# Kernel optimization log

Measured on AMD Instinct MI355X. Metric: run time of the kernel, lower is better.

The kernel has to match this reference:

```python
import jax, jax.numpy as jnp
import numpy as np

D = 256   # d_model
KG = 64   # KG_dim
B, N = 8, 512
EPS = 1e-5

def setup_inputs() -> dict:
    key = jax.random.key(0)
    ks = jax.random.split(key, 20)
    s = 0.05
    return {
        "vectors": jax.random.normal(ks[0], (B, N, D), jnp.float32),
        "KG_matrix": jax.random.normal(ks[1], (B, N, N, KG), jnp.float32),
        "Wq": jax.random.normal(ks[2], (D, D), jnp.float32) * s,
        "bq": jnp.zeros((D,), jnp.float32),
        "Wk": jax.random.normal(ks[3], (D, D), jnp.float32) * s,
        "bk": jnp.zeros((D,), jnp.float32),
        "Wv": jax.random.normal(ks[4], (D, D), jnp.float32) * s,
        "bv": jnp.zeros((D,), jnp.float32),
        "Wkg": jax.random.normal(ks[5], (KG, KG), jnp.float32) * s,
        "bkg": jnp.zeros((KG,), jnp.float32),
        "fc_w": jax.random.normal(ks[6], (2 * D + KG,), jnp.float32) * s,
        "fc_b": jnp.zeros((), jnp.float32),
        "ln_g": jnp.ones((D,), jnp.float32),
        "ln_b": jnp.zeros((D,), jnp.float32),
        "W1": jax.random.normal(ks[7], (D, D), jnp.float32) * s,
        "b1": jnp.zeros((D,), jnp.float32),
        "W2": jax.random.normal(ks[8], (D, D), jnp.float32) * s,
        "b2": jnp.zeros((D,), jnp.float32),
        "Wo": jax.random.normal(ks[9], (D, D), jnp.float32) * s,  # out_proj (unused in fwd, kept for parity)
        "bo": jnp.zeros((D,), jnp.float32),
    }

def reference(vectors, KG_matrix, Wq, bq, Wk, bk, Wv, bv, Wkg, bkg,
              fc_w, fc_b, ln_g, ln_b, W1, b1, W2, b2, Wo, bo):
    # projections + relu activation (self.activation == relu)
    q = jax.nn.relu(vectors @ Wq + bq)          # [B,N,D]
    k = jax.nn.relu(vectors @ Wk + bk)          # [B,N,D]
    v = jax.nn.relu(vectors @ Wv + bv)          # [B,N,D]
    kg = jax.nn.relu(KG_matrix @ Wkg + bkg)     # [B,N,N,KG]

    # fc over concat([q_i, k_j, kg_ij]) decomposed: score_ij = q_i.wq + k_j.wk + kg_ij.wkg + b
    wq_p, wk_p, wkg_p = fc_w[:D], fc_w[D:2 * D], fc_w[2 * D:]
    sq = q @ wq_p                               # [B,N]
    sk = k @ wk_p                               # [B,N]
    skg = jnp.einsum('bijc,c->bij', kg, wkg_p)  # [B,N,N]
    scores = sq[:, :, None] + sk[:, None, :] + skg + fc_b

    attn_weights = jax.nn.softmax(jax.nn.leaky_relu(scores), axis=-1)  # [B,N,N]
    attn_output = jnp.einsum('bij,bjd->bid', attn_weights, v)          # [B,N,D]

    src = v + attn_output  # dropout = identity at inference
    # LayerNorm
    mu = jnp.mean(src, axis=-1, keepdims=True)
    var = jnp.var(src, axis=-1, keepdims=True)
    src2 = (src - mu) * jax.lax.rsqrt(var + EPS) * ln_g + ln_b
    # FFN with leaky_relu (as in the torch code)
    src2 = jax.nn.leaky_relu(src2 @ W1 + b1) @ W2 + b2
    return src + src2
```

## Files before the change

### kernel.cpp

```cpp
#include <hip/hip_runtime.h>
#include <hip/hip_bf16.h>

#define DD 256
#define NJ 512
#define KGC 64

__device__ inline float wave_reduce_sum(float v) {
  #pragma unroll
  for (int off = 32; off > 0; off >>= 1) v += __shfl_xor(v, off, 64);
  return v;
}
__device__ inline float wave_reduce_max(float v) {
  #pragma unroll
  for (int off = 32; off > 0; off >>= 1) v = fmaxf(v, __shfl_xor(v, off, 64));
  return v;
}

__global__ __launch_bounds__(256) void k_qkv(
    const float* __restrict__ vec,
    const float* __restrict__ Wq, const float* __restrict__ bq,
    const float* __restrict__ Wk, const float* __restrict__ bk,
    const float* __restrict__ Wv, const float* __restrict__ bv,
    const float* __restrict__ fc_w,
    float* __restrict__ v_out, float* __restrict__ sq_out, float* __restrict__ sk_out)
{
  const int R = 8;
  const int r0 = blockIdx.x * R;
  const int tid = threadIdx.x;
  const int lane = tid & 63, wid = tid >> 6;

  __shared__ float sx[R * DD];
  __shared__ float redq[R][4], redk[R][4];

  for (int idx = tid; idx < R * DD; idx += 256)
    sx[idx] = vec[(size_t)r0 * DD + idx];
  __syncthreads();

  const int d = tid;
  float aq[R], ak[R], av[R];
  const float bqd = bq[d], bkd = bk[d], bvd = bv[d];
  #pragma unroll
  for (int r = 0; r < R; r++) { aq[r] = bqd; ak[r] = bkd; av[r] = bvd; }

  for (int k = 0; k < DD; k++) {
    float wq = Wq[k * DD + d], wk = Wk[k * DD + d], wv = Wv[k * DD + d];
    #pragma unroll
    for (int r = 0; r < R; r++) {
      float x = sx[r * DD + k];
      aq[r] = fmaf(x, wq, aq[r]);
      ak[r] = fmaf(x, wk, ak[r]);
      av[r] = fmaf(x, wv, av[r]);
    }
  }

  const float fq = fc_w[d], fk = fc_w[DD + d];
  #pragma unroll
  for (int r = 0; r < R; r++) {
    float vq = fmaxf(aq[r], 0.f) * fq;
    float vk = fmaxf(ak[r], 0.f) * fk;
    vq = wave_reduce_sum(vq);
    vk = wave_reduce_sum(vk);
    if (lane == 0) { redq[r][wid] = vq; redk[r][wid] = vk; }
    v_out[(size_t)(r0 + r) * DD + d] = fmaxf(av[r], 0.f);
  }
  __syncthreads();
  if (tid < R) {
    sq_out[r0 + tid] = redq[tid][0] + redq[tid][1] + redq[tid][2] + redq[tid][3];
  } else if (tid < 2 * R) {
    int r = tid - R;
    sk_out[r0 + r] = redk[r][0] + redk[r][1] + redk[r][2] + redk[r][3];
  }
}

__global__ __launch_bounds__(512) void k_attn(
    const float* __restrict__ KG,
    const float* __restrict__ Wkg, const float* __restrict__ bkg,
    const float* __restrict__ fc_w, const float* __restrict__ fc_b,
    const float* __restrict__ sq, const float* __restrict__ sk,
    const float* __restrict__ v, float* __restrict__ src_out)
{
  const int IT = 4;
  const int row0 = blockIdx.x * IT;
  const int b = row0 >> 9;
  const int tid = threadIdx.x;
  const int lane = tid & 63, wid = tid >> 6;

  __shared__ float sw[IT][NJ];
  __shared__ float smax[8], ssum[8];
  __shared__ float sacc[512];

  const float* wkgp = fc_w + 2 * DD;
  const float fcb = fc_b[0];
  const int j = tid;
  const float skj = sk[b * NJ + j];

  #pragma unroll 1
  for (int ii = 0; ii < IT; ii++) {
    const int i = row0 + ii;
    const float* kgrow = KG + ((size_t)i * NJ + j) * KGC;
    float y[KGC];
    #pragma unroll
    for (int c = 0; c < KGC; c++) y[c] = bkg[c];

    #pragma unroll 1
    for (int cp = 0; cp < KGC; cp += 8) {
      float4 x0 = *(const float4*)(kgrow + cp);
      float4 x1 = *(const float4*)(kgrow + cp + 4);
      float x[8] = {x0.x, x0.y, x0.z, x0.w, x1.x, x1.y, x1.z, x1.w};
      #pragma unroll
      for (int u = 0; u < 8; u++) {
        #pragma unroll
        for (int c = 0; c < KGC; c++)
          y[c] = fmaf(x[u], Wkg[(cp + u) * KGC + c], y[c]);
      }
    }
    float skg = 0.f;
    #pragma unroll
    for (int c = 0; c < KGC; c++) skg = fmaf(fmaxf(y[c], 0.f), wkgp[c], skg);

    float sc = sq[i] + skj + skg + fcb;
    sc = sc > 0.f ? sc : 0.01f * sc;
    sw[ii][j] = sc;
  }
  __syncthreads();

  #pragma unroll 1
  for (int ii = 0; ii < IT; ii++) {
    float x = sw[ii][tid];
    float m = wave_reduce_max(x);
    if (lane == 0) smax[wid] = m;
    __syncthreads();
    m = smax[0];
    #pragma unroll
    for (int w = 1; w < 8; w++) m = fmaxf(m, smax[w]);
    float e = __expf(x - m);
    float s = wave_reduce_sum(e);
    if (lane == 0) ssum[wid] = s;
    __syncthreads();
    s = 0.f;
    #pragma unroll
    for (int w = 0; w < 8; w++) s += ssum[w];
    sw[ii][tid] = e * (1.0f / s);
    __syncthreads();
  }

  const int d = tid & 255;
  const int half = tid >> 8;
  float acc[IT] = {0.f, 0.f, 0.f, 0.f};
  const float* vb = v + (size_t)b * NJ * DD;
  for (int jj = 0; jj < NJ / 2; jj++) {
    int jv = (half << 8) + jj;
    float vv = vb[(size_t)jv * DD + d];
    #pragma unroll
    for (int ii = 0; ii < IT; ii++) acc[ii] = fmaf(sw[ii][jv], vv, acc[ii]);
  }
  #pragma unroll 1
  for (int ii = 0; ii < IT; ii++) {
    sacc[tid] = acc[ii];
    __syncthreads();
    if (tid < 256) {
      float s = sacc[tid] + sacc[tid + 256];
      size_t o = (size_t)(row0 + ii) * DD + tid;
      src_out[o] = v[o] + s;
    }
    __syncthreads();
  }
}

__global__ __launch_bounds__(256) void k_mlp(
    const float* __restrict__ src,
    const float* __restrict__ ln_g, const float* __restrict__ ln_b,
    const float* __restrict__ W1, const float* __restrict__ b1,
    const float* __restrict__ W2, const float* __restrict__ b2,
    float* __restrict__ out)
{
  const int R = 8;
  const int r0 = blockIdx.x * R;
  const int tid = threadIdx.x;
  const int lane = tid & 63, wid = tid >> 6;

  __shared__ float sx[R * DD];
  __shared__ float h1[R * DD];
  __shared__ float smu[R], srs[R];

  for (int idx = tid; idx < R * DD; idx += 256)
    sx[idx] = src[(size_t)r0 * DD + idx];
  __syncthreads();

  for (int r = wid; r < R; r += 4) {
    float s = 0.f, s2 = 0.f;
    #pragma unroll
    for (int u = 0; u < DD / 64; u++) {
      float x = sx[r * DD + u * 64 + lane];
      s += x;
      s2 = fmaf(x, x, s2);
    }
    s = wave_reduce_sum(s);
    s2 = wave_reduce_sum(s2);
    if (lane == 0) {
      float mu = s * (1.f / DD);
      float var = s2 * (1.f / DD) - mu * mu;
      smu[r] = mu;
      srs[r] = rsqrtf(var + 1e-5f);
    }
  }
  __syncthreads();
  for (int idx = tid; idx < R * DD; idx += 256) {
    int r = idx >> 8, k = idx & 255;
    sx[idx] = (sx[idx] - smu[r]) * srs[r] * ln_g[k] + ln_b[k];
  }
  __syncthreads();

  const int d = tid;
  float a1[R];
  const float b1d = b1[d];
  #pragma unroll
  for (int r = 0; r < R; r++) a1[r] = b1d;
  for (int k = 0; k < DD; k++) {
    float w = W1[k * DD + d];
    #pragma unroll
    for (int r = 0; r < R; r++) a1[r] = fmaf(sx[r * DD + k], w, a1[r]);
  }
  #pragma unroll
  for (int r = 0; r < R; r++) {
    float hv = a1[r];
    h1[r * DD + d] = hv > 0.f ? hv : 0.01f * hv;
  }
  __syncthreads();

  float a2[R];
  const float b2d = b2[d];
  #pragma unroll
  for (int r = 0; r < R; r++) a2[r] = b2d;
  for (int k = 0; k < DD; k++) {
    float w = W2[k * DD + d];
    #pragma unroll
    for (int r = 0; r < R; r++) a2[r] = fmaf(h1[r * DD + k], w, a2[r]);
  }
  #pragma unroll
  for (int r = 0; r < R; r++) {
    size_t o = (size_t)(r0 + r) * DD + d;
    out[o] = src[o] + a2[r];
  }
}

extern "C" void kernel_launch(void* const* d_in, const int* in_sizes, int n_in,
                              void* d_out, int out_size, void* d_ws, size_t ws_size,
                              hipStream_t stream) {
  const float* vectors = (const float*)d_in[0];
  const float* KG      = (const float*)d_in[1];
  const float* Wq      = (const float*)d_in[2];
  const float* bq      = (const float*)d_in[3];
  const float* Wk      = (const float*)d_in[4];
  const float* bk      = (const float*)d_in[5];
  const float* Wv      = (const float*)d_in[6];
  const float* bv      = (const float*)d_in[7];
  const float* Wkg     = (const float*)d_in[8];
  const float* bkg     = (const float*)d_in[9];
  const float* fc_w    = (const float*)d_in[10];
  const float* fc_b    = (const float*)d_in[11];
  const float* ln_g    = (const float*)d_in[12];
  const float* ln_b    = (const float*)d_in[13];
  const float* W1      = (const float*)d_in[14];
  const float* b1      = (const float*)d_in[15];
  const float* W2      = (const float*)d_in[16];
  const float* b2      = (const float*)d_in[17];

  float* out = (float*)d_out;

  const int ROWS = 8 * 512;
  char* ws = (char*)d_ws;
  float* v_ws  = (float*)ws;
  float* sq_ws = (float*)(ws + (size_t)ROWS * DD * 4);
  float* sk_ws = sq_ws + ROWS;
  float* src_ws = sk_ws + ROWS;

  k_qkv<<<ROWS / 8, 256, 0, stream>>>(vectors, Wq, bq, Wk, bk, Wv, bv, fc_w,
                                      v_ws, sq_ws, sk_ws);
  k_attn<<<ROWS / 4, 512, 0, stream>>>(KG, Wkg, bkg, fc_w, fc_b,
                                       sq_ws, sk_ws, v_ws, src_ws);
  k_mlp<<<ROWS / 8, 256, 0, stream>>>(src_ws, ln_g, ln_b, W1, b1, W2, b2, out);
}
```

Before: 931.7 us.

## Compute KG projection with bf16 MFMA and restructure attention softmax/PV

The per-pair KG projection (64x64 matmul per (i,j)) moves from scalar FP32 FMAs to bf16 MFMA 16x16x32 instructions. Weights are held in registers as bf16 fragments and the fc reduction is done with lane shuffles. The attention kernel is reorganised to 256 threads with transposed softmax weights and float4 PV accumulation. The QKV and MLP kernels read activations as vectors instead of scalars. Rounding KG inputs and weights to bf16 adds precision loss to the scores.

```diff
diff --git a/kernel.cpp b/kernel.cpp
--- a/kernel.cpp
+++ b/kernel.cpp
@@ -5,6 +5,9 @@
 #define NJ 512
 #define KGC 64
 
+typedef float f32x4 __attribute__((ext_vector_type(4)));
+typedef __bf16 bf16x8 __attribute__((ext_vector_type(8)));
+
 __device__ inline float wave_reduce_sum(float v) {
   #pragma unroll
   for (int off = 32; off > 0; off >>= 1) v += __shfl_xor(v, off, 64);
@@ -14,6 +17,13 @@
   #pragma unroll
   for (int off = 32; off > 0; off >>= 1) v = fmaxf(v, __shfl_xor(v, off, 64));
   return v;
+}
+
+__device__ inline __bf16 bf16rne(float x) {
+  unsigned u = __builtin_bit_cast(unsigned, x);
+  u += 0x7fffu + ((u >> 16) & 1u);
+  unsigned short h = (unsigned short)(u >> 16);
+  return __builtin_bit_cast(__bf16, h);
 }
 
 __global__ __launch_bounds__(256) void k_qkv(
@@ -29,12 +39,7 @@
   const int tid = threadIdx.x;
   const int lane = tid & 63, wid = tid >> 6;
 
-  __shared__ float sx[R * DD];
   __shared__ float redq[R][4], redk[R][4];
-
-  for (int idx = tid; idx < R * DD; idx += 256)
-    sx[idx] = vec[(size_t)r0 * DD + idx];
-  __syncthreads();
 
   const int d = tid;
   float aq[R], ak[R], av[R];
@@ -42,14 +47,23 @@
   #pragma unroll
   for (int r = 0; r < R; r++) { aq[r] = bqd; ak[r] = bkd; av[r] = bvd; }
 
-  for (int k = 0; k < DD; k++) {
-    float wq = Wq[k * DD + d], wk = Wk[k * DD + d], wv = Wv[k * DD + d];
-    #pragma unroll
-    for (int r = 0; r < R; r++) {
-      float x = sx[r * DD + k];
-      aq[r] = fmaf(x, wq, aq[r]);
-      ak[r] = fmaf(x, wk, ak[r]);
-      av[r] = fmaf(x, wv, av[r]);
+  const float* xb = vec + (size_t)r0 * DD;
+
+  for (int k = 0; k < DD; k += 4) {
+    f32x4 xr[R];
+    #pragma unroll
+    for (int r = 0; r < R; r++) xr[r] = *(const f32x4*)&xb[r * DD + k];
+    #pragma unroll
+    for (int u = 0; u < 4; u++) {
+      float wq = Wq[(k + u) * DD + d];
+      float wk = Wk[(k + u) * DD + d];
+      float wv = Wv[(k + u) * DD + d];
+      #pragma unroll
+      for (int r = 0; r < R; r++) {
+        aq[r] = fmaf(xr[r][u], wq, aq[r]);
+        ak[r] = fmaf(xr[r][u], wk, ak[r]);
+        av[r] = fmaf(xr[r][u], wv, av[r]);
+      }
     }
   }
 
@@ -72,7 +86,7 @@
   }
 }
 
-__global__ __launch_bounds__(512) void k_attn(
+__global__ __launch_bounds__(256) void k_attn(
     const float* __restrict__ KG,
     const float* __restrict__ Wkg, const float* __restrict__ bkg,
     const float* __restrict__ fc_w, const float* __restrict__ fc_b,
@@ -84,86 +98,133 @@
   const int b = row0 >> 9;
   const int tid = threadIdx.x;
   const int lane = tid & 63, wid = tid >> 6;
-
-  __shared__ float sw[IT][NJ];
-  __shared__ float smax[8], ssum[8];
-  __shared__ float sacc[512];
+  const int quad = lane >> 4, col = lane & 15;
+
+  __shared__ __align__(16) float swT[NJ * IT];
+  __shared__ float smax[4][IT], ssum[4][IT];
+  __shared__ __align__(16) f32x4 red[4][IT][64];
 
   const float* wkgp = fc_w + 2 * DD;
+  bf16x8 bfr[4][2];
+  float bkgv[4], wkgv[4];
+  #pragma unroll
+  for (int nt = 0; nt < 4; nt++) {
+    bkgv[nt] = bkg[nt * 16 + col];
+    wkgv[nt] = wkgp[nt * 16 + col];
+    #pragma unroll
+    for (int t = 0; t < 2; t++) {
+      #pragma unroll
+      for (int j = 0; j < 8; j++)
+        bfr[nt][t][j] = bf16rne(Wkg[(t * 32 + quad * 8 + j) * KGC + nt * 16 + col]);
+    }
+  }
   const float fcb = fc_b[0];
-  const int j = tid;
-  const float skj = sk[b * NJ + j];
 
   #pragma unroll 1
   for (int ii = 0; ii < IT; ii++) {
-    const int i = row0 + ii;
-    const float* kgrow = KG + ((size_t)i * NJ + j) * KGC;
-    float y[KGC];
-    #pragma unroll
-    for (int c = 0; c < KGC; c++) y[c] = bkg[c];
-
+    const float* Ab = KG + (size_t)(row0 + ii) * NJ * KGC;
     #pragma unroll 1
-    for (int cp = 0; cp < KGC; cp += 8) {
-      float4 x0 = *(const float4*)(kgrow + cp);
-      float4 x1 = *(const float4*)(kgrow + cp + 4);
-      float x[8] = {x0.x, x0.y, x0.z, x0.w, x1.x, x1.y, x1.z, x1.w};
-      #pragma unroll
-      for (int u = 0; u < 8; u++) {
+    for (int mi = 0; mi < 8; mi++) {
+      const int m0 = (wid * 8 + mi) * 16;
+      const float* ar = Ab + (size_t)(m0 + col) * KGC + quad * 8;
+      float4 p0 = *(const float4*)(ar);
+      float4 p1 = *(const float4*)(ar + 4);
+      float4 p2 = *(const float4*)(ar + 32);
+      float4 p3 = *(const float4*)(ar + 36);
+      bf16x8 a0, a1;
+      a0[0] = bf16rne(p0.x); a0[1] = bf16rne(p0.y); a0[2] = bf16rne(p0.z); a0[3] = bf16rne(p0.w);
+      a0[4] = bf16rne(p1.x); a0[5] = bf16rne(p1.y); a0[6] = bf16rne(p1.z); a0[7] = bf16rne(p1.w);
+      a1[0] = bf16rne(p2.x); a1[1] = bf16rne(p2.y); a1[2] = bf16rne(p2.z); a1[3] = bf16rne(p2.w);
+      a1[4] = bf16rne(p3.x); a1[5] = bf16rne(p3.y); a1[6] = bf16rne(p3.z); a1[7] = bf16rne(p3.w);
+
+      f32x4 acc[4];
+      #pragma unroll
+      for (int nt = 0; nt < 4; nt++) {
+        acc[nt] = (f32x4){0.f, 0.f, 0.f, 0.f};
+        acc[nt] = __builtin_amdgcn_mfma_f32_16x16x32_bf16(a0, bfr[nt][0], acc[nt], 0, 0, 0);
+        acc[nt] = __builtin_amdgcn_mfma_f32_16x16x32_bf16(a1, bfr[nt][1], acc[nt], 0, 0, 0);
+      }
+
+      float part[4];
+      #pragma unroll
+      for (int reg = 0; reg < 4; reg++) {
+        float s = 0.f;
         #pragma unroll
-        for (int c = 0; c < KGC; c++)
-          y[c] = fmaf(x[u], Wkg[(cp + u) * KGC + c], y[c]);
-      }
-    }
-    float skg = 0.f;
-    #pragma unroll
-    for (int c = 0; c < KGC; c++) skg = fmaf(fmaxf(y[c], 0.f), wkgp[c], skg);
-
-    float sc = sq[i] + skj + skg + fcb;
-    sc = sc > 0.f ? sc : 0.01f * sc;
-    sw[ii][j] = sc;
-  }
-  __syncthreads();
-
-  #pragma unroll 1
-  for (int ii = 0; ii < IT; ii++) {
-    float x = sw[ii][tid];
-    float m = wave_reduce_max(x);
-    if (lane == 0) smax[wid] = m;
+        for (int nt = 0; nt < 4; nt++)
+          s += fmaxf(acc[nt][reg] + bkgv[nt], 0.f) * wkgv[nt];
+        part[reg] = s;
+      }
+      #pragma unroll
+      for (int off = 1; off < 16; off <<= 1) {
+        #pragma unroll
+        for (int reg = 0; reg < 4; reg++)
+          part[reg] += __shfl_xor(part[reg], off, 64);
+      }
+      if (col == 0) {
+        #pragma unroll
+        for (int reg = 0; reg < 4; reg++)
+          swT[(m0 + quad * 4 + reg) * IT + ii] = part[reg];
+      }
+    }
+  }
+  __syncthreads();
+
+  {
+    const float sk0 = sk[b * NJ + tid];
+    const float sk1 = sk[b * NJ + tid + 256];
+    float x0[IT], x1[IT];
+    #pragma unroll
+    for (int ii = 0; ii < IT; ii++) {
+      const float sqi = sq[row0 + ii];
+      float a = swT[tid * IT + ii] + sk0 + sqi + fcb;
+      float c = swT[(tid + 256) * IT + ii] + sk1 + sqi + fcb;
+      a = a > 0.f ? a : 0.01f * a;
+      c = c > 0.f ? c : 0.01f * c;
+      x0[ii] = a; x1[ii] = c;
+      float m = wave_reduce_max(fmaxf(a, c));
+      if (lane == 0) smax[wid][ii] = m;
+    }
     __syncthreads();
-    m = smax[0];
-    #pragma unroll
-    for (int w = 1; w < 8; w++) m = fmaxf(m, smax[w]);
-    float e = __expf(x - m);
-    float s = wave_reduce_sum(e);
-    if (lane == 0) ssum[wid] = s;
+    #pragma unroll
+    for (int ii = 0; ii < IT; ii++) {
+      float m = fmaxf(fmaxf(smax[0][ii], smax[1][ii]), fmaxf(smax[2][ii], smax[3][ii]));
+      float e0 = __expf(x0[ii] - m), e1 = __expf(x1[ii] - m);
+      x0[ii] = e0; x1[ii] = e1;
+      float s = wave_reduce_sum(e0 + e1);
+      if (lane == 0) ssum[wid][ii] = s;
+    }
     __syncthreads();
-    s = 0.f;
-    #pragma unroll
-    for (int w = 0; w < 8; w++) s += ssum[w];
-    sw[ii][tid] = e * (1.0f / s);
+    #pragma unroll
+    for (int ii = 0; ii < IT; ii++) {
+      float s = ssum[0][ii] + ssum[1][ii] + ssum[2][ii] + ssum[3][ii];
+      float iv = 1.f / s;
+      swT[tid * IT + ii] = x0[ii] * iv;
+      swT[(tid + 256) * IT + ii] = x1[ii] * iv;
+    }
     __syncthreads();
   }
 
-  const int d = tid & 255;
-  const int half = tid >> 8;
-  float acc[IT] = {0.f, 0.f, 0.f, 0.f};
-  const float* vb = v + (size_t)b * NJ * DD;
-  for (int jj = 0; jj < NJ / 2; jj++) {
-    int jv = (half << 8) + jj;
-    float vv = vb[(size_t)jv * DD + d];
-    #pragma unroll
-    for (int ii = 0; ii < IT; ii++) acc[ii] = fmaf(sw[ii][jv], vv, acc[ii]);
-  }
-  #pragma unroll 1
-  for (int ii = 0; ii < IT; ii++) {
-    sacc[tid] = acc[ii];
+  {
+    const float* vb = v + (size_t)b * NJ * DD;
+    f32x4 pacc[IT];
+    #pragma unroll
+    for (int ii = 0; ii < IT; ii++) pacc[ii] = (f32x4){0.f, 0.f, 0.f, 0.f};
+    const int j0 = wid * 128;
+    for (int jj = 0; jj < 128; jj++) {
+      const int jv = j0 + jj;
+      f32x4 wv = *(const f32x4*)&swT[jv * IT];
+      f32x4 vv = *(const f32x4*)&vb[(size_t)jv * DD + lane * 4];
+      #pragma unroll
+      for (int ii = 0; ii < IT; ii++) pacc[ii] += wv[ii] * vv;
+    }
+    #pragma unroll
+    for (int ii = 0; ii < IT; ii++) red[wid][ii][lane] = pacc[ii];
     __syncthreads();
-    if (tid < 256) {
-      float s = sacc[tid] + sacc[tid + 256];
-      size_t o = (size_t)(row0 + ii) * DD + tid;
-      src_out[o] = v[o] + s;
-    }
-    __syncthreads();
+    const int ii = tid >> 6, l = tid & 63;
+    f32x4 s = red[0][ii][l] + red[1][ii][l] + red[2][ii][l] + red[3][ii][l];
+    const size_t o = (size_t)(row0 + ii) * DD + l * 4;
+    f32x4 vres = *(const f32x4*)&v[o];
+    *(f32x4*)&src_out[o] = vres + s;
   }
 }
 
@@ -179,8 +240,8 @@
   const int tid = threadIdx.x;
   const int lane = tid & 63, wid = tid >> 6;
 
-  __shared__ float sx[R * DD];
-  __shared__ float h1[R * DD];
+  __shared__ __align__(16) float sx[R * DD];
+  __shared__ __align__(16) float h1[R * DD];
   __shared__ float smu[R], srs[R];
 
   for (int idx = tid; idx < R * DD; idx += 256)
@@ -216,10 +277,16 @@
   const float b1d = b1[d];
   #pragma unroll
   for (int r = 0; r < R; r++) a1[r] = b1d;
-  for (int k = 0; k < DD; k++) {
-    float w = W1[k * DD + d];
-    #pragma unroll
-    for (int r = 0; r < R; r++) a1[r] = fmaf(sx[r * DD + k], w, a1[r]);
+  for (int k = 0; k < DD; k += 4) {
+    f32x4 xr[R];
+    #pragma unroll
+    for (int r = 0; r < R; r++) xr[r] = *(const f32x4*)&sx[r * DD + k];
+    #pragma unroll
+    for (int u = 0; u < 4; u++) {
+      float w = W1[(k + u) * DD + d];
+      #pragma unroll
+      for (int r = 0; r < R; r++) a1[r] = fmaf(xr[r][u], w, a1[r]);
+    }
   }
   #pragma unroll
   for (int r = 0; r < R; r++) {
@@ -232,10 +299,16 @@
   const float b2d = b2[d];
   #pragma unroll
   for (int r = 0; r < R; r++) a2[r] = b2d;
-  for (int k = 0; k < DD; k++) {
-    float w = W2[k * DD + d];
-    #pragma unroll
-    for (int r = 0; r < R; r++) a2[r] = fmaf(h1[r * DD + k], w, a2[r]);
+  for (int k = 0; k < DD; k += 4) {
+    f32x4 xr[R];
+    #pragma unroll
+    for (int r = 0; r < R; r++) xr[r] = *(const f32x4*)&h1[r * DD + k];
+    #pragma unroll
+    for (int u = 0; u < 4; u++) {
+      float w = W2[(k + u) * DD + d];
+      #pragma unroll
+      for (int r = 0; r < R; r++) a2[r] = fmaf(xr[r][u], w, a2[r]);
+    }
   }
   #pragma unroll
   for (int r = 0; r < R; r++) {
@@ -277,7 +350,7 @@
 
   k_qkv<<<ROWS / 8, 256, 0, stream>>>(vectors, Wq, bq, Wk, bk, Wv, bv, fc_w,
                                       v_ws, sq_ws, sk_ws);
-  k_attn<<<ROWS / 4, 512, 0, stream>>>(KG, Wkg, bkg, fc_w, fc_b,
+  k_attn<<<ROWS / 4, 256, 0, stream>>>(KG, Wkg, bkg, fc_w, fc_b,
                                        sq_ws, sk_ws, v_ws, src_ws);
   k_mlp<<<ROWS / 8, 256, 0, stream>>>(src_ws, ln_g, ln_b, W1, b1, W2, b2, out);
 }
```

New measurement: 839.5 us. -9.9%, faster.
